# Kernel tuning notes

Hardware: AMD Instinct MI355X
Metric: run time of the kernel (lower is better)

## Reference

```python
import jax, jax.numpy as jnp
import numpy as np

H = 768


def _glorot(key, shape):
    fan_in = shape[-1]
    return jax.random.normal(key, shape, dtype=jnp.float32) / np.sqrt(fan_in)


def setup_inputs() -> dict:
    key = jax.random.key(0)
    ks = jax.random.split(key, 12)
    B, L, K, Lg = 8, 256, 32, 128
    return {
        "x": jax.random.normal(ks[0], (B, L, H), dtype=jnp.float32),
        "s": jax.random.normal(ks[1], (B, K, H), dtype=jnp.float32),
        "g": jax.random.normal(ks[2], (B, Lg, H), dtype=jnp.float32),
        "Wq": _glorot(ks[3], (H, H)),
        "bq": jnp.zeros((H,), jnp.float32),
        "Wkv": _glorot(ks[4], (2 * H, H)),
        "bkv": jnp.zeros((2 * H,), jnp.float32),
        "Wg1": _glorot(ks[5], (H, 2 * H)),
        "bg1": jnp.zeros((H,), jnp.float32),
        "Wg2": _glorot(ks[6], (H, 2 * H)),
        "bg2": jnp.zeros((H,), jnp.float32),
    }


def _gate(xb, yb, W, b):
    # gate = sigmoid(Linear(concat([x, y], -1))) using split-weight trick:
    # concat([x,y]) @ W.T = x @ Wx.T + y @ Wy.T  (avoids materializing 2H concat)
    Wx, Wy = W[:, :H], W[:, H:]
    gate = jax.nn.sigmoid(jnp.einsum('blkh,oh->blko', xb, Wx)
                          + jnp.einsum('blkh,oh->blko', yb, Wy) + b)
    return gate * xb + (1.0 - gate) * yb


def reference(x, s, g, Wq, bq, Wkv, bkv, Wg1, bg1, Wg2, bg2):
    B, L, _ = x.shape
    K = s.shape[1]
    q = jnp.einsum('blh,oh->blo', x, Wq) + bq                    # (B,L,H)
    kv = jnp.einsum('bmh,oh->bmo', g, Wkv) + bkv                 # (B,Lg,2H)
    k, v = kv[..., :H], kv[..., H:]
    scores = jnp.einsum('blh,bmh->blm', q, k) / np.sqrt(H)       # (B,L,Lg)
    scores = jax.nn.softmax(scores, axis=-1)
    gctx = jnp.einsum('blm,bmh->blh', scores, v)                 # (B,L,H)
    # broadcast to (B,L,K,H)
    gb = jnp.broadcast_to(gctx[:, :, None, :], (B, L, K, H))
    hb = jnp.broadcast_to(x[:, :, None, :], (B, L, K, H))
    sb = jnp.broadcast_to(s[:, None, :, :], (B, L, K, H))
    h = _gate(hb, gb, Wg1, bg1)
    h = _gate(h, sb, Wg2, bg2)
    return h
```

## Files before the change

### kernel.cpp

```cpp
#include <hip/hip_runtime.h>
#include <math.h>

#define Hd 768
#define Bb 8
#define Ll 256
#define Kk 32
#define LG 128

using half4 = __attribute__((ext_vector_type(4))) _Float16;
using half8 = __attribute__((ext_vector_type(8))) _Float16;
using f32x4 = __attribute__((ext_vector_type(4))) float;

__device__ __forceinline__ float sigm(float z) { return 1.f / (1.f + __expf(-z)); }

struct ConvArgs {
    const float* src[8];
    _Float16*    dst[8];
    int cum[9];
    int sstr[8];
    int dstr[8];
    int rl[8];
};

__global__ __launch_bounds__(256) void conv_multi(ConvArgs a) {
    int c = blockIdx.x * 256 + threadIdx.x;
    if (c >= a.cum[8]) return;
    int s = 0;
    while (c >= a.cum[s + 1]) ++s;
    const int lc  = c - a.cum[s];
    const unsigned cpr = (unsigned)(a.rl[s] >> 3);
    const unsigned row = (unsigned)lc / cpr;
    const int col = (lc - (int)(row * cpr)) * 8;
    const float* sp = a.src[s] + (size_t)row * a.sstr[s] + col;
    float4 v0 = *(const float4*)sp;
    float4 v1 = *(const float4*)(sp + 4);
    half8 h;
    h[0] = (_Float16)v0.x; h[1] = (_Float16)v0.y; h[2] = (_Float16)v0.z; h[3] = (_Float16)v0.w;
    h[4] = (_Float16)v1.x; h[5] = (_Float16)v1.y; h[6] = (_Float16)v1.z; h[7] = (_Float16)v1.w;
    *(half8*)(a.dst[s] + (size_t)row * a.dstr[s] + col) = h;
}


struct G3Desc {
    const _Float16* A;
    const _Float16* W;
    const float* bias;
    void* o0;
    void* o1;
    int lda, ldw, mode, nbx;
};
struct G3Args { G3Desc d[3]; int cum[4]; };

__global__ __launch_bounds__(256) void gemm3(G3Args ga) {
    __shared__ _Float16 As[64][72];
    __shared__ _Float16 Ws[64][72];

    const int t    = threadIdx.x;
    const int w    = t >> 6;
    const int lane = t & 63;
    const int quad = lane >> 4;
    const int l16  = lane & 15;

    int s = 0;
    const int bid = blockIdx.x;
    while (bid >= ga.cum[s + 1]) ++s;
    const int local = bid - ga.cum[s];
    const int nbx   = ga.d[s].nbx;
    const int by    = local / nbx;
    const int bx    = local - by * nbx;
    const int bm    = by * 64;
    const int bn    = bx * 64;
    const _Float16* A = ga.d[s].A;
    const _Float16* W = ga.d[s].W;
    const int lda = ga.d[s].lda;
    const int ldw = ga.d[s].ldw;

    const int sr = t >> 3;
    const int sk = (t & 7) * 8;

    f32x4 acc[4] = {};

    half8 av[2], wv[2];
    #pragma unroll
    for (int i = 0; i < 2; ++i) {
        av[i] = *(const half8*)(A + (size_t)(bm + i * 32 + sr) * lda + sk);
        wv[i] = *(const half8*)(W + (size_t)(bn + i * 32 + sr) * ldw + sk);
    }

    for (int k0 = 0; k0 < 768; k0 += 64) {
        __syncthreads();
        #pragma unroll
        for (int i = 0; i < 2; ++i) {
            *(half8*)&As[i * 32 + sr][sk] = av[i];
            *(half8*)&Ws[i * 32 + sr][sk] = wv[i];
        }
        __syncthreads();
        if (k0 + 64 < 768) {
            #pragma unroll
            for (int i = 0; i < 2; ++i) {
                av[i] = *(const half8*)(A + (size_t)(bm + i * 32 + sr) * lda + k0 + 64 + sk);
                wv[i] = *(const half8*)(W + (size_t)(bn + i * 32 + sr) * ldw + k0 + 64 + sk);
            }
        }
        __builtin_amdgcn_sched_barrier(0);
        #pragma unroll
        for (int kk = 0; kk < 2; ++kk) {
            half8 af = *(const half8*)&As[w * 16 + l16][kk * 32 + quad * 8];
            #pragma unroll
            for (int j = 0; j < 4; ++j) {
                half8 bf = *(const half8*)&Ws[j * 16 + l16][kk * 32 + quad * 8];
                acc[j] = __builtin_amdgcn_mfma_f32_16x16x32_f16(af, bf, acc[j], 0, 0, 0);
            }
        }
    }

    const int mode = ga.d[s].mode;
    const float* bias = ga.d[s].bias;
    #pragma unroll
    for (int j = 0; j < 4; ++j) {
        const int col  = bn + j * 16 + l16;
        const int row0 = bm + w * 16 + quad * 4;
        const float bv = bias ? bias[col] : 0.f;
        if (mode == 0) {
            _Float16* C2 = (_Float16*)ga.d[s].o0;
            #pragma unroll
            for (int r = 0; r < 4; ++r)
                C2[(size_t)(row0 + r) * 768 + col] = (_Float16)(acc[j][r] + bv);
        } else if (mode == 1) {
            _Float16* K16  = (_Float16*)ga.d[s].o0;
            _Float16* VT16 = (_Float16*)ga.d[s].o1;
            if (col < 768) {
                #pragma unroll
                for (int r = 0; r < 4; ++r)
                    K16[(size_t)(row0 + r) * 768 + col] = (_Float16)(acc[j][r] + bv);
            } else {
                const int b = row0 >> 7, h = col - 768, m0 = row0 & 127;
                half4 hv;
                #pragma unroll
                for (int r = 0; r < 4; ++r) hv[r] = (_Float16)(acc[j][r] + bv);
                *(half4*)(VT16 + ((size_t)(b * 768 + h)) * 128 + m0) = hv;
            }
        } else {
            float* C = (float*)ga.d[s].o0;
            #pragma unroll
            for (int r = 0; r < 4; ++r)
                C[(size_t)(row0 + r) * 768 + col] = acc[j][r] + bv;
        }
    }
}

__global__ __launch_bounds__(256) void attn_scores_sm(
    const _Float16* __restrict__ Q, const _Float16* __restrict__ Kt,
    _Float16* __restrict__ P)
{
    __shared__ _Float16 As[64][72];
    __shared__ _Float16 Ws[128][72];

    const int t    = threadIdx.x;
    const int w    = t >> 6;
    const int lane = t & 63;
    const int quad = lane >> 4;
    const int l16  = lane & 15;
    const int z    = blockIdx.y;
    const int bm   = blockIdx.x * 64;
    const _Float16* A = Q  + (size_t)z * 256 * 768 + (size_t)bm * 768;
    const _Float16* W = Kt + (size_t)z * 128 * 768;

    const int sr = t >> 3;
    const int sk = (t & 7) * 8;

    f32x4 acc[8] = {};

    half8 av[2], wv[4];
    #pragma unroll
    for (int i = 0; i < 2; ++i)
        av[i] = *(const half8*)(A + (size_t)(i * 32 + sr) * 768 + sk);
    #pragma unroll
    for (int i = 0; i < 4; ++i)
        wv[i] = *(const half8*)(W + (size_t)(i * 32 + sr) * 768 + sk);

    for (int k0 = 0; k0 < 768; k0 += 64) {
        __syncthreads();
        #pragma unroll
        for (int i = 0; i < 2; ++i) *(half8*)&As[i * 32 + sr][sk] = av[i];
        #pragma unroll
        for (int i = 0; i < 4; ++i) *(half8*)&Ws[i * 32 + sr][sk] = wv[i];
        __syncthreads();
        if (k0 + 64 < 768) {
            #pragma unroll
            for (int i = 0; i < 2; ++i)
                av[i] = *(const half8*)(A + (size_t)(i * 32 + sr) * 768 + k0 + 64 + sk);
            #pragma unroll
            for (int i = 0; i < 4; ++i)
                wv[i] = *(const half8*)(W + (size_t)(i * 32 + sr) * 768 + k0 + 64 + sk);
        }
        __builtin_amdgcn_sched_barrier(0);
        #pragma unroll
        for (int kk = 0; kk < 2; ++kk) {
            half8 af = *(const half8*)&As[w * 16 + l16][kk * 32 + quad * 8];
            #pragma unroll
            for (int j = 0; j < 8; ++j) {
                half8 bf = *(const half8*)&Ws[j * 16 + l16][kk * 32 + quad * 8];
                acc[j] = __builtin_amdgcn_mfma_f32_16x16x32_f16(af, bf, acc[j], 0, 0, 0);
            }
        }
    }

    const float scale = 0.03608439182435161f;
    #pragma unroll
    for (int r = 0; r < 4; ++r) {
        float v[8];
        float mx = -1e30f;
        #pragma unroll
        for (int j = 0; j < 8; ++j) { v[j] = acc[j][r] * scale; mx = fmaxf(mx, v[j]); }
        #pragma unroll
        for (int off = 8; off; off >>= 1) mx = fmaxf(mx, __shfl_xor(mx, off, 16));
        float sum = 0.f;
        #pragma unroll
        for (int j = 0; j < 8; ++j) { v[j] = __expf(v[j] - mx); sum += v[j]; }
        #pragma unroll
        for (int off = 8; off; off >>= 1) sum += __shfl_xor(sum, off, 16);
        const float inv = 1.f / sum;
        const int row = bm + w * 16 + quad * 4 + r;
        _Float16* Pr = P + (size_t)z * 256 * 128 + (size_t)row * 128;
        #pragma unroll
        for (int j = 0; j < 8; ++j) Pr[j * 16 + l16] = (_Float16)(v[j] * inv);
    }
}

__global__ __launch_bounds__(256) void gemm_gctx(
    const _Float16* __restrict__ A, int lda, long sA,
    const _Float16* __restrict__ W, int ldw, long sW,
    float* __restrict__ C, int ldc, long sC,
    _Float16* __restrict__ C2, int ldc2, long sC2)
{
    __shared__ _Float16 As[64][72];
    __shared__ _Float16 Ws[64][72];

    const int t    = threadIdx.x;
    const int w    = t >> 6;
    const int lane = t & 63;
    const int quad = lane >> 4;
    const int l16  = lane & 15;
    const int bm   = blockIdx.y * 64;
    const int bn   = blockIdx.x * 64;
    const int z    = blockIdx.z;
    A += (size_t)z * sA;
    W += (size_t)z * sW;

    const int sr = t >> 3;
    const int sk = (t & 7) * 8;

    f32x4 acc[4] = {};

    half8 av[2], wv[2];
    #pragma unroll
    for (int i = 0; i < 2; ++i) {
        av[i] = *(const half8*)(A + (size_t)(bm + i * 32 + sr) * lda + sk);
        wv[i] = *(const half8*)(W + (size_t)(bn + i * 32 + sr) * ldw + sk);
    }

    for (int k0 = 0; k0 < 128; k0 += 64) {
        __syncthreads();
        #pragma unroll
        for (int i = 0; i < 2; ++i) {
            *(half8*)&As[i * 32 + sr][sk] = av[i];
            *(half8*)&Ws[i * 32 + sr][sk] = wv[i];
        }
        __syncthreads();
        if (k0 + 64 < 128) {
            #pragma unroll
            for (int i = 0; i < 2; ++i) {
                av[i] = *(const half8*)(A + (size_t)(bm + i * 32 + sr) * lda + k0 + 64 + sk);
                wv[i] = *(const half8*)(W + (size_t)(bn + i * 32 + sr) * ldw + k0 + 64 + sk);
            }
        }
        __builtin_amdgcn_sched_barrier(0);
        #pragma unroll
        for (int kk = 0; kk < 2; ++kk) {
            half8 af = *(const half8*)&As[w * 16 + l16][kk * 32 + quad * 8];
            #pragma unroll
            for (int j = 0; j < 4; ++j) {
                half8 bf = *(const half8*)&Ws[j * 16 + l16][kk * 32 + quad * 8];
                acc[j] = __builtin_amdgcn_mfma_f32_16x16x32_f16(af, bf, acc[j], 0, 0, 0);
            }
        }
    }

    #pragma unroll
    for (int j = 0; j < 4; ++j) {
        const int col  = bn + j * 16 + l16;
        const int row0 = bm + w * 16 + quad * 4;
        #pragma unroll
        for (int r = 0; r < 4; ++r) {
            const float v = acc[j][r];
            const size_t rr = (size_t)(row0 + r);
            C[(size_t)z * sC + rr * ldc + col] = v;
            C2[(size_t)z * sC2 + rr * ldc2 + col] = (_Float16)v;
        }
    }
}

__global__ __launch_bounds__(256) void gemm_gate1(
    const _Float16* __restrict__ A,
    const _Float16* __restrict__ W,
    const float* __restrict__ bias,
    const float* __restrict__ X,
    const float* __restrict__ GC,
    float* __restrict__ H1,
    _Float16* __restrict__ H16)
{
    __shared__ _Float16 As[64][72];
    __shared__ _Float16 Ws[64][72];

    const int t    = threadIdx.x;
    const int w    = t >> 6;
    const int lane = t & 63;
    const int quad = lane >> 4;
    const int l16  = lane & 15;
    const int bm   = blockIdx.y * 64;
    const int bn   = blockIdx.x * 64;

    const int sr = t >> 3;
    const int sk = (t & 7) * 8;

    f32x4 acc[4] = {};

    half8 av[2], wv[2];
    #pragma unroll
    for (int i = 0; i < 2; ++i) {
        av[i] = *(const half8*)(A + (size_t)(bm + i * 32 + sr) * 1536 + sk);
        wv[i] = *(const half8*)(W + (size_t)(bn + i * 32 + sr) * 1536 + sk);
    }

    for (int k0 = 0; k0 < 1536; k0 += 64) {
        __syncthreads();
        #pragma unroll
        for (int i = 0; i < 2; ++i) {
            *(half8*)&As[i * 32 + sr][sk] = av[i];
            *(half8*)&Ws[i * 32 + sr][sk] = wv[i];
        }
        __syncthreads();
        if (k0 + 64 < 1536) {
            #pragma unroll
            for (int i = 0; i < 2; ++i) {
                av[i] = *(const half8*)(A + (size_t)(bm + i * 32 + sr) * 1536 + k0 + 64 + sk);
                wv[i] = *(const half8*)(W + (size_t)(bn + i * 32 + sr) * 1536 + k0 + 64 + sk);
            }
        }
        __builtin_amdgcn_sched_barrier(0);
        #pragma unroll
        for (int kk = 0; kk < 2; ++kk) {
            half8 af = *(const half8*)&As[w * 16 + l16][kk * 32 + quad * 8];
            #pragma unroll
            for (int j = 0; j < 4; ++j) {
                half8 bf = *(const half8*)&Ws[j * 16 + l16][kk * 32 + quad * 8];
                acc[j] = __builtin_amdgcn_mfma_f32_16x16x32_f16(af, bf, acc[j], 0, 0, 0);
            }
        }
    }

    #pragma unroll
    for (int j = 0; j < 4; ++j) {
        const int col  = bn + j * 16 + l16;
        const int row0 = bm + w * 16 + quad * 4;
        const float bv = bias[col];
        #pragma unroll
        for (int r = 0; r < 4; ++r) {
            const size_t off = (size_t)(row0 + r) * 768 + col;
            const float g = sigm(acc[j][r] + bv);
            const float o = g * X[off] + (1.f - g) * GC[off];
            H1[off]  = o;
            H16[off] = (_Float16)o;
        }
    }
}

__global__ __launch_bounds__(256) void gemm_final(
    const _Float16* __restrict__ A,
    const _Float16* __restrict__ W,
    const float* __restrict__ bias,
    const float* __restrict__ Ebuf,
    const float* __restrict__ Sbuf,
    const float* __restrict__ H1,
    float* __restrict__ out)
{
    __shared__ union {
        struct { _Float16 As[64][72]; _Float16 Ws[64][72]; } a;
        float Ds[64][76];
    } u;
    __shared__ float Es[32][64];
    __shared__ float Ss[32][64];

    const int t    = threadIdx.x;
    const int w    = t >> 6;
    const int lane = t & 63;
    const int quad = lane >> 4;
    const int l16  = lane & 15;
    const int bm   = blockIdx.y * 64;
    const int bn   = blockIdx.x * 64;
    const int bK   = (bm >> 8) * 32;

    const int sr = t >> 3;
    const int sk = (t & 7) * 8;

    #pragma unroll
    for (int i = 0; i < 2; ++i) {
        const int idx = t + i * 256;
        const int k = idx >> 4, c = (idx & 15) * 4;
        *(float4*)&Es[k][c] = *(const float4*)(Ebuf + (size_t)(bK + k) * 768 + bn + c);
        *(float4*)&Ss[k][c] = *(const float4*)(Sbuf + (size_t)(bK + k) * 768 + bn + c);
    }

    f32x4 acc[4] = {};

    half8 av[2], wv[2];
    #pragma unroll
    for (int i = 0; i < 2; ++i) {
        av[i] = *(const half8*)(A + (size_t)(bm + i * 32 + sr) * 768 + sk);
        wv[i] = *(const half8*)(W + (size_t)(bn + i * 32 + sr) * 768 + sk);
    }

    for (int k0 = 0; k0 < 768; k0 += 64) {
        __syncthreads();
        #pragma unroll
        for (int i = 0; i < 2; ++i) {
            *(half8*)&u.a.As[i * 32 + sr][sk] = av[i];
            *(half8*)&u.a.Ws[i * 32 + sr][sk] = wv[i];
        }
        __syncthreads();
        if (k0 + 64 < 768) {
            #pragma unroll
            for (int i = 0; i < 2; ++i) {
                av[i] = *(const half8*)(A + (size_t)(bm + i * 32 + sr) * 768 + k0 + 64 + sk);
                wv[i] = *(const half8*)(W + (size_t)(bn + i * 32 + sr) * 768 + k0 + 64 + sk);
            }
        }
        __builtin_amdgcn_sched_barrier(0);
        #pragma unroll
        for (int kk = 0; kk < 2; ++kk) {
            half8 af = *(const half8*)&u.a.As[w * 16 + l16][kk * 32 + quad * 8];
            #pragma unroll
            for (int j = 0; j < 4; ++j) {
                half8 bf = *(const half8*)&u.a.Ws[j * 16 + l16][kk * 32 + quad * 8];
                acc[j] = __builtin_amdgcn_mfma_f32_16x16x32_f16(af, bf, acc[j], 0, 0, 0);
            }
        }
    }

    __syncthreads();
    #pragma unroll
    for (int j = 0; j < 4; ++j) {
        const int col = j * 16 + l16;
        const float bv = bias[bn + col];
        #pragma unroll
        for (int r = 0; r < 4; ++r)
            u.Ds[w * 16 + quad * 4 + r][col] = acc[j][r] + bv;
    }
    __syncthreads();

    const int c  = (t & 15) * 4;
    const int r0 = (t >> 4) * 4;
    float4 d[4], h[4];
    #pragma unroll
    for (int rr = 0; rr < 4; ++rr) {
        d[rr] = *(const float4*)&u.Ds[r0 + rr][c];
        h[rr] = *(const float4*)(H1 + (size_t)(bm + r0 + rr) * 768 + bn + c);
    }
    float* ob = out + (size_t)(bm + r0) * 32 * 768 + bn + c;
    for (int k = 0; k < 32; ++k) {
        const float4 e  = *(const float4*)&Es[k][c];
        const float4 sv = *(const float4*)&Ss[k][c];
        #pragma unroll
        for (int rr = 0; rr < 4; ++rr) {
            float4 o; float g;
            g = sigm(d[rr].x + e.x); o.x = g * h[rr].x + (1.f - g) * sv.x;
            g = sigm(d[rr].y + e.y); o.y = g * h[rr].y + (1.f - g) * sv.y;
            g = sigm(d[rr].z + e.z); o.z = g * h[rr].z + (1.f - g) * sv.z;
            g = sigm(d[rr].w + e.w); o.w = g * h[rr].w + (1.f - g) * sv.w;
            *(float4*)(ob + (size_t)(rr * 32 + k) * 768) = o;
        }
    }
}

extern "C" void kernel_launch(void* const* d_in, const int* in_sizes, int n_in,
                              void* d_out, int out_size, void* d_ws, size_t ws_size,
                              hipStream_t stream) {
    const float* x   = (const float*)d_in[0];
    const float* s   = (const float*)d_in[1];
    const float* g   = (const float*)d_in[2];
    const float* Wq  = (const float*)d_in[3];
    const float* bq  = (const float*)d_in[4];
    const float* Wkv = (const float*)d_in[5];
    const float* bkv = (const float*)d_in[6];
    const float* Wg1 = (const float*)d_in[7];
    const float* bg1 = (const float*)d_in[8];
    const float* Wg2 = (const float*)d_in[9];
    const float* bg2 = (const float*)d_in[10];

    char* w = (char*)d_ws;
    _Float16* P16    = (_Float16*)(w + 0);
    _Float16* xg16   = (_Float16*)(w + 524288);
    _Float16* g16    = (_Float16*)(w + 6815744);
    _Float16* s16    = (_Float16*)(w + 8388608);
    _Float16* q16    = (_Float16*)(w + 8781824);
    _Float16* k16    = (_Float16*)(w + 11927552);
    _Float16* vT16   = (_Float16*)(w + 13500416);
    _Float16* Wq16   = (_Float16*)(w + 15073280);
    _Float16* Wkv16  = (_Float16*)(w + 16252928);
    _Float16* Wg116  = (_Float16*)(w + 18612224);
    _Float16* Wg2a16 = (_Float16*)(w + 20971520);
    _Float16* Wg2b16 = (_Float16*)(w + 22151168);
    float*    bufE   = (float*)(w + 23330816);
    float*    bufC   = (float*)(w + 24117248);
    float*    bufB   = (float*)(w + 30408704);
    _Float16* h116   = (_Float16*)(w + 36700160);
    float* out = (float*)d_out;

    const dim3 blk(256);

    ConvArgs ca;
    ca.src[0] = x;         ca.dst[0] = xg16;   ca.sstr[0] = 768;  ca.dstr[0] = 1536; ca.rl[0] = 768;
    ca.src[1] = g;         ca.dst[1] = g16;    ca.sstr[1] = 768;  ca.dstr[1] = 768;  ca.rl[1] = 768;
    ca.src[2] = s;         ca.dst[2] = s16;    ca.sstr[2] = 768;  ca.dstr[2] = 768;  ca.rl[2] = 768;
    ca.src[3] = Wq;        ca.dst[3] = Wq16;   ca.sstr[3] = 768;  ca.dstr[3] = 768;  ca.rl[3] = 768;
    ca.src[4] = Wkv;       ca.dst[4] = Wkv16;  ca.sstr[4] = 768;  ca.dstr[4] = 768;  ca.rl[4] = 768;
    ca.src[5] = Wg1;       ca.dst[5] = Wg116;  ca.sstr[5] = 1536; ca.dstr[5] = 1536; ca.rl[5] = 1536;
    ca.src[6] = Wg2;       ca.dst[6] = Wg2a16; ca.sstr[6] = 1536; ca.dstr[6] = 768;  ca.rl[6] = 768;
    ca.src[7] = Wg2 + 768; ca.dst[7] = Wg2b16; ca.sstr[7] = 1536; ca.dstr[7] = 768;  ca.rl[7] = 768;
    ca.cum[0] = 0;      ca.cum[1] = 196608; ca.cum[2] = 294912; ca.cum[3] = 319488;
    ca.cum[4] = 393216; ca.cum[5] = 540672; ca.cum[6] = 688128; ca.cum[7] = 761856;
    ca.cum[8] = 835584;
    conv_multi<<<dim3(3264), blk, 0, stream>>>(ca);

    G3Args ga = {};
    ga.d[0] = { xg16, Wq16,   bq,      (void*)q16,  nullptr,     1536, 768, 0, 12 };
    ga.d[1] = { g16,  Wkv16,  bkv,     (void*)k16,  (void*)vT16, 768,  768, 1, 24 };
    ga.d[2] = { s16,  Wg2b16, nullptr, (void*)bufE, nullptr,     768,  768, 2, 12 };
    ga.cum[0] = 0; ga.cum[1] = 384; ga.cum[2] = 768; ga.cum[3] = 816;
    gemm3<<<dim3(816), blk, 0, stream>>>(ga);

    attn_scores_sm<<<dim3(4, 8), blk, 0, stream>>>(q16, k16, P16);

    gemm_gctx<<<dim3(12, 4, 8), blk, 0, stream>>>(
        P16, 128, 256L * 128, vT16, 128, 768L * 128,
        bufC, 768, 256L * 768, xg16 + 768, 1536, 256L * 1536);

    gemm_gate1<<<dim3(12, 32), blk, 0, stream>>>(
        xg16, Wg116, bg1, x, bufC, bufB, h116);

    gemm_final<<<dim3(12, 32), blk, 0, stream>>>(
        h116, Wg2a16, bg2, bufE, s, bufB, out);
}
```

Baseline: 311.4 us.

## Fuse attention softmax with PV GEMM and double-buffer LDS in GEMM kernels

Merges the score/softmax kernel and the P·V GEMM into one kernel that keeps the probability tile in shared memory and streams V^T through double-buffered LDS, removing the P workspace round trip and one launch. All GEMM-style kernels also move to double-buffered shared tiles with a single barrier per k-step. The fused attention kernel runs only 32 blocks and loops serially over 12 output column groups, so the PV part loses parallelism that the separate 384-block GEMM had.

```diff
diff --git a/kernel.cpp b/kernel.cpp
--- a/kernel.cpp
+++ b/kernel.cpp
@@ -1,11 +1,5 @@
 #include <hip/hip_runtime.h>
 #include <math.h>
-
-#define Hd 768
-#define Bb 8
-#define Ll 256
-#define Kk 32
-#define LG 128
 
 using half4 = __attribute__((ext_vector_type(4))) _Float16;
 using half8 = __attribute__((ext_vector_type(8))) _Float16;
@@ -52,8 +46,8 @@
 struct G3Args { G3Desc d[3]; int cum[4]; };
 
 __global__ __launch_bounds__(256) void gemm3(G3Args ga) {
-    __shared__ _Float16 As[64][72];
-    __shared__ _Float16 Ws[64][72];
+    __shared__ _Float16 As[2][64][72];
+    __shared__ _Float16 Ws[2][64][72];
 
     const int t    = threadIdx.x;
     const int w    = t >> 6;
@@ -79,39 +73,51 @@
     const int sk = (t & 7) * 8;
 
     f32x4 acc[4] = {};
-
     half8 av[2], wv[2];
+
     #pragma unroll
     for (int i = 0; i < 2; ++i) {
         av[i] = *(const half8*)(A + (size_t)(bm + i * 32 + sr) * lda + sk);
         wv[i] = *(const half8*)(W + (size_t)(bn + i * 32 + sr) * ldw + sk);
     }
-
-    for (int k0 = 0; k0 < 768; k0 += 64) {
+    #pragma unroll
+    for (int i = 0; i < 2; ++i) {
+        *(half8*)&As[0][i * 32 + sr][sk] = av[i];
+        *(half8*)&Ws[0][i * 32 + sr][sk] = wv[i];
+    }
+    #pragma unroll
+    for (int i = 0; i < 2; ++i) {
+        av[i] = *(const half8*)(A + (size_t)(bm + i * 32 + sr) * lda + 64 + sk);
+        wv[i] = *(const half8*)(W + (size_t)(bn + i * 32 + sr) * ldw + 64 + sk);
+    }
+    __syncthreads();
+
+    for (int it = 0; it < 12; ++it) {
+        const int cur = it & 1;
+        #pragma unroll
+        for (int kk = 0; kk < 2; ++kk) {
+            half8 af = *(const half8*)&As[cur][w * 16 + l16][kk * 32 + quad * 8];
+            #pragma unroll
+            for (int j = 0; j < 4; ++j) {
+                half8 bf = *(const half8*)&Ws[cur][j * 16 + l16][kk * 32 + quad * 8];
+                acc[j] = __builtin_amdgcn_mfma_f32_16x16x32_f16(af, bf, acc[j], 0, 0, 0);
+            }
+        }
+        if (it + 1 < 12) {
+            #pragma unroll
+            for (int i = 0; i < 2; ++i) {
+                *(half8*)&As[cur ^ 1][i * 32 + sr][sk] = av[i];
+                *(half8*)&Ws[cur ^ 1][i * 32 + sr][sk] = wv[i];
+            }
+        }
+        if (it + 2 < 12) {
+            #pragma unroll
+            for (int i = 0; i < 2; ++i) {
+                av[i] = *(const half8*)(A + (size_t)(bm + i * 32 + sr) * lda + (it + 2) * 64 + sk);
+                wv[i] = *(const half8*)(W + (size_t)(bn + i * 32 + sr) * ldw + (it + 2) * 64 + sk);
+            }
+        }
         __syncthreads();
-        #pragma unroll
-        for (int i = 0; i < 2; ++i) {
-            *(half8*)&As[i * 32 + sr][sk] = av[i];
-            *(half8*)&Ws[i * 32 + sr][sk] = wv[i];
-        }
-        __syncthreads();
-        if (k0 + 64 < 768) {
-            #pragma unroll
-            for (int i = 0; i < 2; ++i) {
-                av[i] = *(const half8*)(A + (size_t)(bm + i * 32 + sr) * lda + k0 + 64 + sk);
-                wv[i] = *(const half8*)(W + (size_t)(bn + i * 32 + sr) * ldw + k0 + 64 + sk);
-            }
-        }
-        __builtin_amdgcn_sched_barrier(0);
-        #pragma unroll
-        for (int kk = 0; kk < 2; ++kk) {
-            half8 af = *(const half8*)&As[w * 16 + l16][kk * 32 + quad * 8];
-            #pragma unroll
-            for (int j = 0; j < 4; ++j) {
-                half8 bf = *(const half8*)&Ws[j * 16 + l16][kk * 32 + quad * 8];
-                acc[j] = __builtin_amdgcn_mfma_f32_16x16x32_f16(af, bf, acc[j], 0, 0, 0);
-            }
-        }
     }
 
     const int mode = ga.d[s].mode;
@@ -149,20 +155,23 @@
     }
 }
 
-__global__ __launch_bounds__(256) void attn_scores_sm(
+__global__ __launch_bounds__(256) void attn_pv(
     const _Float16* __restrict__ Q, const _Float16* __restrict__ Kt,
-    _Float16* __restrict__ P)
+    const _Float16* __restrict__ Vt16,
+    float* __restrict__ bufC, _Float16* __restrict__ xg16)
 {
-    __shared__ _Float16 As[64][72];
-    __shared__ _Float16 Ws[128][72];
+    __shared__ union {
+        struct { _Float16 Qs[2][64][72]; _Float16 Ks[2][128][72]; } qk;
+        struct { _Float16 Ps[64][136]; _Float16 Vs[2][64][136]; } pv;
+    } sh;
 
     const int t    = threadIdx.x;
     const int w    = t >> 6;
     const int lane = t & 63;
     const int quad = lane >> 4;
     const int l16  = lane & 15;
-    const int z    = blockIdx.y;
-    const int bm   = blockIdx.x * 64;
+    const int z    = blockIdx.x >> 2;
+    const int bm   = (blockIdx.x & 3) * 64;
     const _Float16* A = Q  + (size_t)z * 256 * 768 + (size_t)bm * 768;
     const _Float16* W = Kt + (size_t)z * 128 * 768;
 
@@ -170,40 +179,52 @@
     const int sk = (t & 7) * 8;
 
     f32x4 acc[8] = {};
-
     half8 av[2], wv[4];
+
     #pragma unroll
     for (int i = 0; i < 2; ++i)
         av[i] = *(const half8*)(A + (size_t)(i * 32 + sr) * 768 + sk);
     #pragma unroll
     for (int i = 0; i < 4; ++i)
         wv[i] = *(const half8*)(W + (size_t)(i * 32 + sr) * 768 + sk);
-
-    for (int k0 = 0; k0 < 768; k0 += 64) {
+    #pragma unroll
+    for (int i = 0; i < 2; ++i) *(half8*)&sh.qk.Qs[0][i * 32 + sr][sk] = av[i];
+    #pragma unroll
+    for (int i = 0; i < 4; ++i) *(half8*)&sh.qk.Ks[0][i * 32 + sr][sk] = wv[i];
+    #pragma unroll
+    for (int i = 0; i < 2; ++i)
+        av[i] = *(const half8*)(A + (size_t)(i * 32 + sr) * 768 + 64 + sk);
+    #pragma unroll
+    for (int i = 0; i < 4; ++i)
+        wv[i] = *(const half8*)(W + (size_t)(i * 32 + sr) * 768 + 64 + sk);
+    __syncthreads();
+
+    for (int it = 0; it < 12; ++it) {
+        const int cur = it & 1;
+        #pragma unroll
+        for (int kk = 0; kk < 2; ++kk) {
+            half8 af = *(const half8*)&sh.qk.Qs[cur][w * 16 + l16][kk * 32 + quad * 8];
+            #pragma unroll
+            for (int j = 0; j < 8; ++j) {
+                half8 bf = *(const half8*)&sh.qk.Ks[cur][j * 16 + l16][kk * 32 + quad * 8];
+                acc[j] = __builtin_amdgcn_mfma_f32_16x16x32_f16(af, bf, acc[j], 0, 0, 0);
+            }
+        }
+        if (it + 1 < 12) {
+            #pragma unroll
+            for (int i = 0; i < 2; ++i) *(half8*)&sh.qk.Qs[cur ^ 1][i * 32 + sr][sk] = av[i];
+            #pragma unroll
+            for (int i = 0; i < 4; ++i) *(half8*)&sh.qk.Ks[cur ^ 1][i * 32 + sr][sk] = wv[i];
+        }
+        if (it + 2 < 12) {
+            #pragma unroll
+            for (int i = 0; i < 2; ++i)
+                av[i] = *(const half8*)(A + (size_t)(i * 32 + sr) * 768 + (it + 2) * 64 + sk);
+            #pragma unroll
+            for (int i = 0; i < 4; ++i)
+                wv[i] = *(const half8*)(W + (size_t)(i * 32 + sr) * 768 + (it + 2) * 64 + sk);
+        }
         __syncthreads();
-        #pragma unroll
-        for (int i = 0; i < 2; ++i) *(half8*)&As[i * 32 + sr][sk] = av[i];
-        #pragma unroll
-        for (int i = 0; i < 4; ++i) *(half8*)&Ws[i * 32 + sr][sk] = wv[i];
-        __syncthreads();
-        if (k0 + 64 < 768) {
-            #pragma unroll
-            for (int i = 0; i < 2; ++i)
-                av[i] = *(const half8*)(A + (size_t)(i * 32 + sr) * 768 + k0 + 64 + sk);
-            #pragma unroll
-            for (int i = 0; i < 4; ++i)
-                wv[i] = *(const half8*)(W + (size_t)(i * 32 + sr) * 768 + k0 + 64 + sk);
-        }
-        __builtin_amdgcn_sched_barrier(0);
-        #pragma unroll
-        for (int kk = 0; kk < 2; ++kk) {
-            half8 af = *(const half8*)&As[w * 16 + l16][kk * 32 + quad * 8];
-            #pragma unroll
-            for (int j = 0; j < 8; ++j) {
-                half8 bf = *(const half8*)&Ws[j * 16 + l16][kk * 32 + quad * 8];
-                acc[j] = __builtin_amdgcn_mfma_f32_16x16x32_f16(af, bf, acc[j], 0, 0, 0);
-            }
-        }
     }
 
     const float scale = 0.03608439182435161f;
@@ -221,83 +242,64 @@
         #pragma unroll
         for (int off = 8; off; off >>= 1) sum += __shfl_xor(sum, off, 16);
         const float inv = 1.f / sum;
-        const int row = bm + w * 16 + quad * 4 + r;
-        _Float16* Pr = P + (size_t)z * 256 * 128 + (size_t)row * 128;
-        #pragma unroll
-        for (int j = 0; j < 8; ++j) Pr[j * 16 + l16] = (_Float16)(v[j] * inv);
-    }
-}
-
-__global__ __launch_bounds__(256) void gemm_gctx(
-    const _Float16* __restrict__ A, int lda, long sA,
-    const _Float16* __restrict__ W, int ldw, long sW,
-    float* __restrict__ C, int ldc, long sC,
-    _Float16* __restrict__ C2, int ldc2, long sC2)
-{
-    __shared__ _Float16 As[64][72];
-    __shared__ _Float16 Ws[64][72];
-
-    const int t    = threadIdx.x;
-    const int w    = t >> 6;
-    const int lane = t & 63;
-    const int quad = lane >> 4;
-    const int l16  = lane & 15;
-    const int bm   = blockIdx.y * 64;
-    const int bn   = blockIdx.x * 64;
-    const int z    = blockIdx.z;
-    A += (size_t)z * sA;
-    W += (size_t)z * sW;
-
-    const int sr = t >> 3;
-    const int sk = (t & 7) * 8;
-
-    f32x4 acc[4] = {};
-
-    half8 av[2], wv[2];
-    #pragma unroll
-    for (int i = 0; i < 2; ++i) {
-        av[i] = *(const half8*)(A + (size_t)(bm + i * 32 + sr) * lda + sk);
-        wv[i] = *(const half8*)(W + (size_t)(bn + i * 32 + sr) * ldw + sk);
-    }
-
-    for (int k0 = 0; k0 < 128; k0 += 64) {
+        const int prow = w * 16 + quad * 4 + r;
+        #pragma unroll
+        for (int j = 0; j < 8; ++j)
+            sh.pv.Ps[prow][j * 16 + l16] = (_Float16)(v[j] * inv);
+    }
+
+    const _Float16* Vt = Vt16 + (size_t)z * 768 * 128;
+    float*     Cc = bufC + ((size_t)(z * 256 + bm)) * 768;
+    _Float16*  Xg = xg16 + ((size_t)(z * 256 + bm)) * 1536 + 768;
+
+    const int vrow = t >> 2;
+    const int vcb  = (t & 3) * 32;
+    half8 vv[4];
+    {
+        const _Float16* vp = Vt + (size_t)vrow * 128 + vcb;
+        #pragma unroll
+        for (int i = 0; i < 4; ++i)
+            *(half8*)&sh.pv.Vs[0][vrow][vcb + i * 8] = *(const half8*)(vp + i * 8);
+        const _Float16* vp1 = Vt + (size_t)(64 + vrow) * 128 + vcb;
+        #pragma unroll
+        for (int i = 0; i < 4; ++i) vv[i] = *(const half8*)(vp1 + i * 8);
+    }
+    __syncthreads();
+
+    for (int cg = 0; cg < 12; ++cg) {
+        const int cur = cg & 1;
+        f32x4 a2[4] = {};
+        #pragma unroll
+        for (int kk = 0; kk < 4; ++kk) {
+            half8 af = *(const half8*)&sh.pv.Ps[w * 16 + l16][kk * 32 + quad * 8];
+            #pragma unroll
+            for (int j = 0; j < 4; ++j) {
+                half8 bf = *(const half8*)&sh.pv.Vs[cur][j * 16 + l16][kk * 32 + quad * 8];
+                a2[j] = __builtin_amdgcn_mfma_f32_16x16x32_f16(af, bf, a2[j], 0, 0, 0);
+            }
+        }
+        if (cg + 1 < 12) {
+            #pragma unroll
+            for (int i = 0; i < 4; ++i)
+                *(half8*)&sh.pv.Vs[cur ^ 1][vrow][vcb + i * 8] = vv[i];
+        }
+        if (cg + 2 < 12) {
+            const _Float16* vp = Vt + (size_t)((cg + 2) * 64 + vrow) * 128 + vcb;
+            #pragma unroll
+            for (int i = 0; i < 4; ++i) vv[i] = *(const half8*)(vp + i * 8);
+        }
+        #pragma unroll
+        for (int j = 0; j < 4; ++j) {
+            const int col  = cg * 64 + j * 16 + l16;
+            const int row0 = w * 16 + quad * 4;
+            #pragma unroll
+            for (int r = 0; r < 4; ++r) {
+                const float vvl = a2[j][r];
+                Cc[(size_t)(row0 + r) * 768 + col] = vvl;
+                Xg[(size_t)(row0 + r) * 1536 + col] = (_Float16)vvl;
+            }
+        }
         __syncthreads();
-        #pragma unroll
-        for (int i = 0; i < 2; ++i) {
-            *(half8*)&As[i * 32 + sr][sk] = av[i];
-            *(half8*)&Ws[i * 32 + sr][sk] = wv[i];
-        }
-        __syncthreads();
-        if (k0 + 64 < 128) {
-            #pragma unroll
-            for (int i = 0; i < 2; ++i) {
-                av[i] = *(const half8*)(A + (size_t)(bm + i * 32 + sr) * lda + k0 + 64 + sk);
-                wv[i] = *(const half8*)(W + (size_t)(bn + i * 32 + sr) * ldw + k0 + 64 + sk);
-            }
-        }
-        __builtin_amdgcn_sched_barrier(0);
-        #pragma unroll
-        for (int kk = 0; kk < 2; ++kk) {
-            half8 af = *(const half8*)&As[w * 16 + l16][kk * 32 + quad * 8];
-            #pragma unroll
-            for (int j = 0; j < 4; ++j) {
-                half8 bf = *(const half8*)&Ws[j * 16 + l16][kk * 32 + quad * 8];
-                acc[j] = __builtin_amdgcn_mfma_f32_16x16x32_f16(af, bf, acc[j], 0, 0, 0);
-            }
-        }
-    }
-
-    #pragma unroll
-    for (int j = 0; j < 4; ++j) {
-        const int col  = bn + j * 16 + l16;
-        const int row0 = bm + w * 16 + quad * 4;
-        #pragma unroll
-        for (int r = 0; r < 4; ++r) {
-            const float v = acc[j][r];
-            const size_t rr = (size_t)(row0 + r);
-            C[(size_t)z * sC + rr * ldc + col] = v;
-            C2[(size_t)z * sC2 + rr * ldc2 + col] = (_Float16)v;
-        }
     }
 }
 
@@ -310,8 +312,8 @@
     float* __restrict__ H1,
     _Float16* __restrict__ H16)
 {
-    __shared__ _Float16 As[64][72];
-    __shared__ _Float16 Ws[64][72];
+    __shared__ _Float16 As[2][64][72];
+    __shared__ _Float16 Ws[2][64][72];
 
     const int t    = threadIdx.x;
     const int w    = t >> 6;
@@ -325,39 +327,51 @@
     const int sk = (t & 7) * 8;
 
     f32x4 acc[4] = {};
-
     half8 av[2], wv[2];
+
     #pragma unroll
     for (int i = 0; i < 2; ++i) {
         av[i] = *(const half8*)(A + (size_t)(bm + i * 32 + sr) * 1536 + sk);
         wv[i] = *(const half8*)(W + (size_t)(bn + i * 32 + sr) * 1536 + sk);
     }
-
-    for (int k0 = 0; k0 < 1536; k0 += 64) {
+    #pragma unroll
+    for (int i = 0; i < 2; ++i) {
+        *(half8*)&As[0][i * 32 + sr][sk] = av[i];
+        *(half8*)&Ws[0][i * 32 + sr][sk] = wv[i];
+    }
+    #pragma unroll
+    for (int i = 0; i < 2; ++i) {
+        av[i] = *(const half8*)(A + (size_t)(bm + i * 32 + sr) * 1536 + 64 + sk);
+        wv[i] = *(const half8*)(W + (size_t)(bn + i * 32 + sr) * 1536 + 64 + sk);
+    }
+    __syncthreads();
+
+    for (int it = 0; it < 24; ++it) {
+        const int cur = it & 1;
+        #pragma unroll
+        for (int kk = 0; kk < 2; ++kk) {
+            half8 af = *(const half8*)&As[cur][w * 16 + l16][kk * 32 + quad * 8];
+            #pragma unroll
+            for (int j = 0; j < 4; ++j) {
+                half8 bf = *(const half8*)&Ws[cur][j * 16 + l16][kk * 32 + quad * 8];
+                acc[j] = __builtin_amdgcn_mfma_f32_16x16x32_f16(af, bf, acc[j], 0, 0, 0);
+            }
+        }
+        if (it + 1 < 24) {
+            #pragma unroll
+            for (int i = 0; i < 2; ++i) {
+                *(half8*)&As[cur ^ 1][i * 32 + sr][sk] = av[i];
+                *(half8*)&Ws[cur ^ 1][i * 32 + sr][sk] = wv[i];
+            }
+        }
+        if (it + 2 < 24) {
+            #pragma unroll
+            for (int i = 0; i < 2; ++i) {
+                av[i] = *(const half8*)(A + (size_t)(bm + i * 32 + sr) * 1536 + (it + 2) * 64 + sk);
+                wv[i] = *(const half8*)(W + (size_t)(bn + i * 32 + sr) * 1536 + (it + 2) * 64 + sk);
+            }
+        }
         __syncthreads();
-        #pragma unroll
-        for (int i = 0; i < 2; ++i) {
-            *(half8*)&As[i * 32 + sr][sk] = av[i];
-            *(half8*)&Ws[i * 32 + sr][sk] = wv[i];
-        }
-        __syncthreads();
-        if (k0 + 64 < 1536) {
-            #pragma unroll
-            for (int i = 0; i < 2; ++i) {
-                av[i] = *(const half8*)(A + (size_t)(bm + i * 32 + sr) * 1536 + k0 + 64 + sk);
-                wv[i] = *(const half8*)(W + (size_t)(bn + i * 32 + sr) * 1536 + k0 + 64 + sk);
-            }
-        }
-        __builtin_amdgcn_sched_barrier(0);
-        #pragma unroll
-        for (int kk = 0; kk < 2; ++kk) {
-            half8 af = *(const half8*)&As[w * 16 + l16][kk * 32 + quad * 8];
-            #pragma unroll
-            for (int j = 0; j < 4; ++j) {
-                half8 bf = *(const half8*)&Ws[j * 16 + l16][kk * 32 + quad * 8];
-                acc[j] = __builtin_amdgcn_mfma_f32_16x16x32_f16(af, bf, acc[j], 0, 0, 0);
-            }
-        }
     }
 
     #pragma unroll
@@ -386,7 +400,7 @@
     float* __restrict__ out)
 {
     __shared__ union {
-        struct { _Float16 As[64][72]; _Float16 Ws[64][72]; } a;
+        struct { _Float16 As[2][64][72]; _Float16 Ws[2][64][72]; } a;
         float Ds[64][76];
     } u;
     __shared__ float Es[32][64];
@@ -413,42 +427,53 @@
     }
 
     f32x4 acc[4] = {};
-
     half8 av[2], wv[2];
+
     #pragma unroll
     for (int i = 0; i < 2; ++i) {
         av[i] = *(const half8*)(A + (size_t)(bm + i * 32 + sr) * 768 + sk);
         wv[i] = *(const half8*)(W + (size_t)(bn + i * 32 + sr) * 768 + sk);
     }
-
-    for (int k0 = 0; k0 < 768; k0 += 64) {
+    #pragma unroll
+    for (int i = 0; i < 2; ++i) {
+        *(half8*)&u.a.As[0][i * 32 + sr][sk] = av[i];
+        *(half8*)&u.a.Ws[0][i * 32 + sr][sk] = wv[i];
+    }
+    #pragma unroll
+    for (int i = 0; i < 2; ++i) {
+        av[i] = *(const half8*)(A + (size_t)(bm + i * 32 + sr) * 768 + 64 + sk);
+        wv[i] = *(const half8*)(W + (size_t)(bn + i * 32 + sr) * 768 + 64 + sk);
+    }
+    __syncthreads();
+
+    for (int it = 0; it < 12; ++it) {
+        const int cur = it & 1;
+        #pragma unroll
+        for (int kk = 0; kk < 2; ++kk) {
+            half8 af = *(const half8*)&u.a.As[cur][w * 16 + l16][kk * 32 + quad * 8];
+            #pragma unroll
+            for (int j = 0; j < 4; ++j) {
+                half8 bf = *(const half8*)&u.a.Ws[cur][j * 16 + l16][kk * 32 + quad * 8];
+                acc[j] = __builtin_amdgcn_mfma_f32_16x16x32_f16(af, bf, acc[j], 0, 0, 0);
+            }
+        }
+        if (it + 1 < 12) {
+            #pragma unroll
+            for (int i = 0; i < 2; ++i) {
+                *(half8*)&u.a.As[cur ^ 1][i * 32 + sr][sk] = av[i];
+                *(half8*)&u.a.Ws[cur ^ 1][i * 32 + sr][sk] = wv[i];
+            }
+        }
+        if (it + 2 < 12) {
+            #pragma unroll
+            for (int i = 0; i < 2; ++i) {
+                av[i] = *(const half8*)(A + (size_t)(bm + i * 32 + sr) * 768 + (it + 2) * 64 + sk);
+                wv[i] = *(const half8*)(W + (size_t)(bn + i * 32 + sr) * 768 + (it + 2) * 64 + sk);
+            }
+        }
         __syncthreads();
-        #pragma unroll
-        for (int i = 0; i < 2; ++i) {
-            *(half8*)&u.a.As[i * 32 + sr][sk] = av[i];
-            *(half8*)&u.a.Ws[i * 32 + sr][sk] = wv[i];
-        }
-        __syncthreads();
-        if (k0 + 64 < 768) {
-            #pragma unroll
-            for (int i = 0; i < 2; ++i) {
-                av[i] = *(const half8*)(A + (size_t)(bm + i * 32 + sr) * 768 + k0 + 64 + sk);
-                wv[i] = *(const half8*)(W + (size_t)(bn + i * 32 + sr) * 768 + k0 + 64 + sk);
-            }
-        }
-        __builtin_amdgcn_sched_barrier(0);
-        #pragma unroll
-        for (int kk = 0; kk < 2; ++kk) {
-            half8 af = *(const half8*)&u.a.As[w * 16 + l16][kk * 32 + quad * 8];
-            #pragma unroll
-            for (int j = 0; j < 4; ++j) {
-                half8 bf = *(const half8*)&u.a.Ws[j * 16 + l16][kk * 32 + quad * 8];
-                acc[j] = __builtin_amdgcn_mfma_f32_16x16x32_f16(af, bf, acc[j], 0, 0, 0);
-            }
-        }
-    }
-
-    __syncthreads();
+    }
+
     #pragma unroll
     for (int j = 0; j < 4; ++j) {
         const int col = j * 16 + l16;
@@ -461,11 +486,11 @@
 
     const int c  = (t & 15) * 4;
     const int r0 = (t >> 4) * 4;
-    float4 d[4], h[4];
+    float4 d4[4], h4v[4];
     #pragma unroll
     for (int rr = 0; rr < 4; ++rr) {
-        d[rr] = *(const float4*)&u.Ds[r0 + rr][c];
-        h[rr] = *(const float4*)(H1 + (size_t)(bm + r0 + rr) * 768 + bn + c);
+        d4[rr]  = *(const float4*)&u.Ds[r0 + rr][c];
+        h4v[rr] = *(const float4*)(H1 + (size_t)(bm + r0 + rr) * 768 + bn + c);
     }
     float* ob = out + (size_t)(bm + r0) * 32 * 768 + bn + c;
     for (int k = 0; k < 32; ++k) {
@@ -474,10 +499,10 @@
         #pragma unroll
         for (int rr = 0; rr < 4; ++rr) {
             float4 o; float g;
-            g = sigm(d[rr].x + e.x); o.x = g * h[rr].x + (1.f - g) * sv.x;
-            g = sigm(d[rr].y + e.y); o.y = g * h[rr].y + (1.f - g) * sv.y;
-            g = sigm(d[rr].z + e.z); o.z = g * h[rr].z + (1.f - g) * sv.z;
-            g = sigm(d[rr].w + e.w); o.w = g * h[rr].w + (1.f - g) * sv.w;
+            g = sigm(d4[rr].x + e.x); o.x = g * h4v[rr].x + (1.f - g) * sv.x;
+            g = sigm(d4[rr].y + e.y); o.y = g * h4v[rr].y + (1.f - g) * sv.y;
+            g = sigm(d4[rr].z + e.z); o.z = g * h4v[rr].z + (1.f - g) * sv.z;
+            g = sigm(d4[rr].w + e.w); o.w = g * h4v[rr].w + (1.f - g) * sv.w;
             *(float4*)(ob + (size_t)(rr * 32 + k) * 768) = o;
         }
     }
@@ -499,7 +524,6 @@
     const float* bg2 = (const float*)d_in[10];
 
     char* w = (char*)d_ws;
-    _Float16* P16    = (_Float16*)(w + 0);
     _Float16* xg16   = (_Float16*)(w + 524288);
     _Float16* g16    = (_Float16*)(w + 6815744);
     _Float16* s16    = (_Float16*)(w + 8388608);
@@ -540,11 +564,7 @@
     ga.cum[0] = 0; ga.cum[1] = 384; ga.cum[2] = 768; ga.cum[3] = 816;
     gemm3<<<dim3(816), blk, 0, stream>>>(ga);
 
-    attn_scores_sm<<<dim3(4, 8), blk, 0, stream>>>(q16, k16, P16);
-
-    gemm_gctx<<<dim3(12, 4, 8), blk, 0, stream>>>(
-        P16, 128, 256L * 128, vT16, 128, 768L * 128,
-        bufC, 768, 256L * 768, xg16 + 768, 1536, 256L * 1536);
+    attn_pv<<<dim3(32), blk, 0, stream>>>(q16, k16, vT16, bufC, xg16);
 
     gemm_gate1<<<dim3(12, 32), blk, 0, stream>>>(
         xg16, Wg116, bg1, x, bufC, bufB, h116);
```

Measured after the change: 316.9 us. No clear change (+1.8%).
